# Kernel tuning notes

Measured on AMD Instinct MI355X. Metric: run time of the kernel, lower is better.

## Reference

```python
import jax, jax.numpy as jnp
import numpy as np

B, T, A, P = 128, 128, 16, 4
D, H, Q, QI, V = 256, 512, 128, 512, 64
NUM_TRICKS = 13
SIGNAL_PHASE = 1
# static phase routing: contiguous blocks of T/P positions per phase (phase_mask buffer)
PHASE_ID = (np.arange(T) * P // T).astype(np.int32)
_DECAY = 0.6
_nt_left = NUM_TRICKS - np.arange(NUM_TRICKS, dtype=np.float32)
P_SIGNAL = ((1.0 - _DECAY) / (1.0 - _DECAY ** _nt_left)).astype(np.float32)


def setup_inputs() -> dict:
    key = jax.random.key(0)
    ks = jax.random.split(key, 12)
    a = jax.random.randint(ks[0], (B, T, A, 3), 0, V, dtype=jnp.int32)
    pad = (jax.random.uniform(ks[1], (B, T, A)) < 0.3) & (jnp.arange(A) >= 1)
    valid_actions = jnp.where(pad[..., None], -1, a)
    phase = jnp.broadcast_to(jnp.asarray(PHASE_ID), (B, T)).astype(jnp.int32)
    trick = jax.random.randint(ks[2], (B, T), 0, NUM_TRICKS, dtype=jnp.int32)
    backbone_embed = jax.random.normal(ks[3], (B, T, QI), jnp.float32)
    s = lambda k, shape, fan: jax.random.normal(k, shape, jnp.float32) / np.float32(np.sqrt(fan))
    return dict(
        backbone_embed=backbone_embed, valid_actions=valid_actions, phase=phase, trick=trick,
        emb0=s(ks[4], (V, D), D), emb1=s(ks[5], (V, D), D), emb2=s(ks[6], (V, D), D),
        ln_g=jnp.ones((D,), jnp.float32), ln_b=jnp.zeros((D,), jnp.float32),
        kW1=s(ks[7], (P, D, H), D), kb1=jnp.zeros((P, H), jnp.float32),
        kW2=s(ks[8], (P, H, H), H), kb2=jnp.zeros((P, H), jnp.float32),
        kW3=s(ks[9], (P, H, Q), H), kb3=jnp.zeros((P, Q), jnp.float32),
        qW=s(ks[10], (P, QI, Q), QI), qb=jnp.zeros((P, Q), jnp.float32),
    )


def _forward(backbone_embed, valid_actions, phase, trick,
             emb0, emb1, emb2, ln_g, ln_b,
             kW1, kb1, kW2, kb2, kW3, kb3, qW, qb):
    pid = PHASE_ID  # static (T,) routing -> gather per-position phase params (same math as mask gather/scatter)
    idx = jnp.clip(valid_actions, 0, V - 1)
    x = emb0[idx[..., 0]] + emb1[idx[..., 1]] + emb2[idx[..., 2]]  # (B,T,A,D) action embed
    mu = jnp.mean(x, -1, keepdims=True)
    var = jnp.var(x, -1, keepdims=True)
    x = (x - mu) * jax.lax.rsqrt(var + 1e-5) * ln_g + ln_b  # key LayerNorm
    # phase-branched key MLP (BranchedFF over MLP)
    h = jax.nn.relu(jnp.einsum('btad,tdh->btah', x, kW1[pid]) + kb1[pid][None, :, None, :])
    h = jax.nn.relu(jnp.einsum('btah,thg->btag', h, kW2[pid]) + kb2[pid][None, :, None, :])
    keyv = jnp.einsum('btah,thq->btaq', h, kW3[pid]) + kb3[pid][None, :, None, :]  # (B,T,A,Q)
    # phase-branched query Linear (BranchedFF over Linear)
    query = jnp.einsum('btd,tdq->btq', backbone_embed, qW[pid]) + qb[pid][None]  # (B,T,Q)
    attn = jnp.einsum('btq,btaq->bta', query, keyv) / np.float32(np.sqrt(Q))
    invalid = valid_actions[..., 0] == -1
    attn = jnp.where(invalid, -jnp.inf, attn)
    # no-signal log-weight
    n_valid = jnp.sum(~invalid, -1).astype(attn.dtype)  # (B,T)
    p_s = jnp.asarray(P_SIGNAL)[trick]
    wgt = jnp.log(jnp.maximum((1.0 - p_s) / p_s * (n_valid - 1.0), 1e-5))
    wgt = jnp.where(n_valid == 1.0, 0.0, wgt)
    attn = attn.at[..., 0].add(jnp.where(phase == SIGNAL_PHASE, wgt, 0.0))
    return jax.nn.log_softmax(attn, axis=-1)


def reference(backbone_embed, valid_actions, phase, trick,
              emb0, emb1, emb2, ln_g, ln_b,
              kW1, kb1, kW2, kb2, kW3, kb3, qW, qb):
    return _forward(backbone_embed, valid_actions, phase, trick,
                    emb0, emb1, emb2, ln_g, ln_b,
                    kW1, kb1, kW2, kb2, kW3, kb3, qW, qb)
```

## Files before the change

### kernel.cpp

```cpp
#include <hip/hip_runtime.h>
#include <hip/hip_bf16.h>
#include <cmath>

constexpr int Bc = 128, Tc = 128, Ac = 16;
constexpr int Dc = 256, Hc = 512, Qc = 128, QIc = 512, Vc = 64, NTk = 13;
constexpr float NEG_BIG = -1e30f;
constexpr float ACT_SCALE = 16.f;
constexpr float ACC_SCALE = 1.f / 256.f;
constexpr float ACC_TO_ACT = 1.f / 16.f;

typedef unsigned int uint;
typedef uint uint2v __attribute__((ext_vector_type(2)));
typedef float f32x4 __attribute__((ext_vector_type(4)));

#define MFMA16F8(a, b, c) __builtin_amdgcn_mfma_f32_16x16x32_fp8_fp8(a, b, c, 0, 0, 0)

__device__ __forceinline__ long long u2ll(uint2v v) {
  union { uint2v u; long long l; } x;
  x.u = v;
  return x.l;
}
__device__ __forceinline__ unsigned short f2bfu(float f) {
  __hip_bfloat16 h = __float2bfloat16(f);
  return *(unsigned short*)&h;
}
__device__ __forceinline__ float bf2f(short s) {
  return __uint_as_float(((unsigned)(unsigned short)s) << 16);
}
__device__ __forceinline__ uint pack4_fp8(float a, float b, float c, float d) {
  uint v = 0;
  v = __builtin_amdgcn_cvt_pk_fp8_f32(a, b, v, 0);
  v = __builtin_amdgcn_cvt_pk_fp8_f32(c, d, v, 1);
  return v;
}

__global__ void transform_all(const float* __restrict__ kW1, const float* __restrict__ kW2,
                              const float* __restrict__ kW3, const float* __restrict__ qW,
                              uint2v* __restrict__ kW1f, uint2v* __restrict__ kW2f,
                              uint2v* __restrict__ kW3f, uint2v* __restrict__ qWf) {
  int gid = blockIdx.x * 256 + threadIdx.x;
  const float* W;
  uint2v* dst;
  int NT, KC, N, local;
  if (gid < 65536) {
    W = kW1; dst = kW1f; NT = 32; KC = 8; N = 512; local = gid;
  } else if (gid < 196608) {
    W = kW2; dst = kW2f; NT = 32; KC = 16; N = 512; local = gid - 65536;
  } else if (gid < 229376) {
    W = kW3; dst = kW3f; NT = 8; KC = 16; N = 128; local = gid - 196608;
  } else {
    W = qW; dst = qWf; NT = 8; KC = 16; N = 128; local = gid - 229376;
  }
  int lane = local & 63;
  int frag = local >> 6;
  int kc = frag % KC;
  int rest = frag / KC;
  int nt = rest % NT;
  int p = rest / NT;
  int K = KC * 32;
  int n = nt * 16 + (lane & 15);
  int k0 = kc * 32 + (lane >> 4) * 8;
  const float* src = W + ((size_t)p * K + k0) * N + n;
  float f[8];
#pragma unroll
  for (int j = 0; j < 8; ++j) f[j] = src[(size_t)j * N] * ACT_SCALE;
  uint2v v;
  v.x = pack4_fp8(f[0], f[1], f[2], f[3]);
  v.y = pack4_fp8(f[4], f[5], f[6], f[7]);
  dst[local] = v;
}

template <int KC, int WT, int AT, bool RELU, int OUTMODE, int SIN, int SOUT>
__device__ __forceinline__ void layer16(
    const char* __restrict__ aB, void* __restrict__ o0,
    const uint2v* __restrict__ Wf, const float* __restrict__ bias,
    int wt0, int lane) {
  const int c = lane & 15, q = lane >> 4;
  const char* ap = aB + c * SIN + q * 8;

  f32x4 acc[WT][AT];
#pragma unroll
  for (int wt = 0; wt < WT; ++wt)
#pragma unroll
    for (int at = 0; at < AT; ++at)
#pragma unroll
      for (int r = 0; r < 4; ++r) acc[wt][at][r] = 0.f;

#pragma unroll 1
  for (int kc = 0; kc < KC; ++kc) {
    uint2v bf[AT];
#pragma unroll
    for (int at = 0; at < AT; ++at)
      bf[at] = *(const uint2v*)(ap + at * 16 * SIN + kc * 32);
#pragma unroll
    for (int wt = 0; wt < WT; ++wt) {
      const uint2v* wk = Wf + ((size_t)(wt0 + wt) * KC + kc) * 64;
      uint2v wv = wk[lane];
      long long ww = u2ll(wv);
#pragma unroll
      for (int at = 0; at < AT; ++at)
        acc[wt][at] = MFMA16F8(ww, u2ll(bf[at]), acc[wt][at]);
    }
  }

#pragma unroll
  for (int wt = 0; wt < WT; ++wt) {
    const int nb = (wt0 + wt) * 16 + 4 * q;
    float4 bv = *(const float4*)(bias + nb);
#pragma unroll
    for (int at = 0; at < AT; ++at) {
      const int row = at * 16 + c;
      if (OUTMODE == 0) {
        float s0 = fmaf(acc[wt][at][0], ACC_TO_ACT, bv.x * ACT_SCALE);
        float s1 = fmaf(acc[wt][at][1], ACC_TO_ACT, bv.y * ACT_SCALE);
        float s2 = fmaf(acc[wt][at][2], ACC_TO_ACT, bv.z * ACT_SCALE);
        float s3 = fmaf(acc[wt][at][3], ACC_TO_ACT, bv.w * ACT_SCALE);
        if (RELU) {
          s0 = fmaxf(s0, 0.f); s1 = fmaxf(s1, 0.f);
          s2 = fmaxf(s2, 0.f); s3 = fmaxf(s3, 0.f);
        }
        *(uint*)((char*)o0 + row * SOUT + nb) = pack4_fp8(s0, s1, s2, s3);
      } else if (OUTMODE == 1) {
        float s0 = fmaf(acc[wt][at][0], ACC_SCALE, bv.x);
        float s1 = fmaf(acc[wt][at][1], ACC_SCALE, bv.y);
        float s2 = fmaf(acc[wt][at][2], ACC_SCALE, bv.z);
        float s3 = fmaf(acc[wt][at][3], ACC_SCALE, bv.w);
        uint2v u;
        u.x = ((uint)f2bfu(s1) << 16) | f2bfu(s0);
        u.y = ((uint)f2bfu(s3) << 16) | f2bfu(s2);
        *(uint2v*)((short*)o0 + row * SOUT + nb) = u;
      } else {
        if (c < 4) {
          float4 st;
          st.x = fmaf(acc[wt][at][0], ACC_SCALE, bv.x);
          st.y = fmaf(acc[wt][at][1], ACC_SCALE, bv.y);
          st.z = fmaf(acc[wt][at][2], ACC_SCALE, bv.z);
          st.w = fmaf(acc[wt][at][3], ACC_SCALE, bv.w);
          *(float4*)((float*)o0 + c * SOUT + nb) = st;
        }
      }
    }
  }
}

constexpr int SX = 280;
constexpr int SH = 536;
constexpr int SKV = 136;
constexpr int SQY = 132;

__global__ __launch_bounds__(1024, 8) void policy_main(
    const float* __restrict__ be, const int* __restrict__ va,
    const int* __restrict__ phase, const int* __restrict__ trick,
    const float* __restrict__ emb0, const float* __restrict__ emb1,
    const float* __restrict__ emb2, const float* __restrict__ ln_g,
    const float* __restrict__ ln_b,
    const float* __restrict__ kb1, const float* __restrict__ kb2,
    const float* __restrict__ kb3, const float* __restrict__ qb,
    const uint2v* __restrict__ kW1f, const uint2v* __restrict__ kW2f,
    const uint2v* __restrict__ kW3f, const uint2v* __restrict__ qWf,
    float* __restrict__ out) {
  __shared__ __align__(16) char bufA[64 * SH];
  __shared__ __align__(16) char bufB[64 * SH];
  __shared__ __align__(16) char beAb[16 * SH];
  __shared__ __align__(16) float QYs[4 * SQY];
  __shared__ float attn_s[64];
  __shared__ int inval_s[64];
  __shared__ int ph_s[4], tr_s[4];

  char* Xs = bufA;
  char* H2 = bufA;
  char* H1 = bufB;
  short* KV = (short*)bufB;

  const int tid = threadIdx.x;
  const int w = tid >> 6, lane = tid & 63;
  const int p = blockIdx.x & 3;
  const int g = blockIdx.x >> 2;
  const int b = g >> 3;
  const int t0 = p * 32 + (g & 7) * 4;
  const int bt0 = b * Tc + t0;

  if (tid < 64) {
    inval_s[tid] = (va[((size_t)bt0 * Ac + tid) * 3] == -1);
  } else if (tid < 68) {
    ph_s[tid - 64] = phase[bt0 + tid - 64];
  } else if (tid < 72) {
    tr_s[tid - 68] = trick[bt0 + tid - 68];
  }
  if (tid < 256) {
    int tok = tid >> 6, d0 = (tid & 63) * 8;
    const float* bp = be + ((size_t)bt0 + tok) * QIc + d0;
    uint2v v8;
    v8.x = pack4_fp8(bp[0] * ACT_SCALE, bp[1] * ACT_SCALE, bp[2] * ACT_SCALE, bp[3] * ACT_SCALE);
    v8.y = pack4_fp8(bp[4] * ACT_SCALE, bp[5] * ACT_SCALE, bp[6] * ACT_SCALE, bp[7] * ACT_SCALE);
    *(uint2v*)(beAb + tok * SH + d0) = v8;
  }
  {
    const int r = tid >> 4, part = tid & 15, d0 = part * 16;
    const int* vp = va + ((size_t)bt0 * Ac + r) * 3;
    int i0 = min(max(vp[0], 0), Vc - 1);
    int i1 = min(max(vp[1], 0), Vc - 1);
    int i2 = min(max(vp[2], 0), Vc - 1);
    const float4* e0 = (const float4*)(emb0 + i0 * Dc + d0);
    const float4* e1 = (const float4*)(emb1 + i1 * Dc + d0);
    const float4* e2 = (const float4*)(emb2 + i2 * Dc + d0);
    float xv[16];
    float sum = 0.f, ss = 0.f;
#pragma unroll
    for (int j = 0; j < 4; ++j) {
      float4 v0 = e0[j], v1 = e1[j], v2 = e2[j];
      float4 v;
      v.x = v0.x + v1.x + v2.x; v.y = v0.y + v1.y + v2.y;
      v.z = v0.z + v1.z + v2.z; v.w = v0.w + v1.w + v2.w;
      xv[j * 4 + 0] = v.x; xv[j * 4 + 1] = v.y; xv[j * 4 + 2] = v.z; xv[j * 4 + 3] = v.w;
      sum += v.x + v.y + v.z + v.w;
      ss += v.x * v.x + v.y * v.y + v.z * v.z + v.w * v.w;
    }
    sum += __shfl_xor(sum, 1); sum += __shfl_xor(sum, 2);
    sum += __shfl_xor(sum, 4); sum += __shfl_xor(sum, 8);
    ss += __shfl_xor(ss, 1);   ss += __shfl_xor(ss, 2);
    ss += __shfl_xor(ss, 4);   ss += __shfl_xor(ss, 8);
    const float mu = sum / (float)Dc;
    const float rstd = rsqrtf(ss / (float)Dc - mu * mu + 1e-5f);
    float y[16];
#pragma unroll
    for (int j = 0; j < 16; ++j) {
      int d = d0 + j;
      y[j] = ((xv[j] - mu) * rstd * ln_g[d] + ln_b[d]) * ACT_SCALE;
    }
    uint2v v8;
    v8.x = pack4_fp8(y[0], y[1], y[2], y[3]);
    v8.y = pack4_fp8(y[4], y[5], y[6], y[7]);
    *(uint2v*)(Xs + r * SX + d0) = v8;
    v8.x = pack4_fp8(y[8], y[9], y[10], y[11]);
    v8.y = pack4_fp8(y[12], y[13], y[14], y[15]);
    *(uint2v*)(Xs + r * SX + d0 + 8) = v8;
  }
  __syncthreads();

  layer16<8, 2, 4, true, 0, SX, SH>(Xs, H1, kW1f + (size_t)p * 32 * 8 * 64,
                                    kb1 + p * Hc, w * 2, lane);
  __syncthreads();

  layer16<16, 2, 4, true, 0, SH, SH>(H1, H2, kW2f + (size_t)p * 32 * 16 * 64,
                                     kb2 + p * Hc, w * 2, lane);
  __syncthreads();

  if (w < 8) {
    layer16<16, 1, 4, false, 1, SH, SKV>(H2, KV, kW3f + (size_t)p * 8 * 16 * 64,
                                         kb3 + p * Qc, w, lane);
  } else {
    layer16<16, 1, 1, false, 2, SH, SQY>(beAb, QYs, qWf + (size_t)p * 8 * 16 * 64,
                                         qb + p * Qc, w - 8, lane);
  }
  __syncthreads();

  {
    const int r = tid >> 4, part = tid & 15, tok = r >> 4;
    const short* kp = KV + r * SKV + part * 8;
    const float* qp = QYs + tok * SQY + part * 8;
    float s = 0.f;
#pragma unroll
    for (int j = 0; j < 8; ++j) s += bf2f(kp[j]) * qp[j];
    s += __shfl_xor(s, 1); s += __shfl_xor(s, 2);
    s += __shfl_xor(s, 4); s += __shfl_xor(s, 8);
    if (part == 0) attn_s[r] = s * 0.08838834764831845f;
  }
  __syncthreads();

  if (tid < 4) {
    const int tok = tid;
    const int bt = bt0 + tok;
    float av[Ac];
    int nv = 0;
#pragma unroll
    for (int a = 0; a < Ac; ++a) {
      int iv = inval_s[tok * Ac + a];
      nv += iv ? 0 : 1;
      av[a] = iv ? NEG_BIG : attn_s[tok * Ac + a];
    }
    if (ph_s[tok] == 1) {
      const int nt = NTk - tr_s[tok];
      float dp = 1.f;
      for (int i = 0; i < nt; ++i) dp *= 0.6f;
      const float ps = 0.4f / (1.f - dp);
      float wgt = (nv == 1) ? 0.f : logf(fmaxf((1.f - ps) / ps * ((float)nv - 1.f), 1e-5f));
      av[0] += wgt;
    }
    float m = NEG_BIG;
#pragma unroll
    for (int a = 0; a < Ac; ++a) m = fmaxf(m, av[a]);
    float s = 0.f;
#pragma unroll
    for (int a = 0; a < Ac; ++a) s += expf(av[a] - m);
    const float lse = logf(s) + m;
#pragma unroll
    for (int a = 0; a < Ac; ++a)
      out[bt * Ac + a] = inval_s[tok * Ac + a] ? NEG_BIG : (av[a] - lse);
  }
}

extern "C" void kernel_launch(void* const* d_in, const int* in_sizes, int n_in,
                              void* d_out, int out_size, void* d_ws, size_t ws_size,
                              hipStream_t stream) {
  const float* be   = (const float*)d_in[0];
  const int*   va   = (const int*)d_in[1];
  const int*   ph   = (const int*)d_in[2];
  const int*   tr   = (const int*)d_in[3];
  const float* emb0 = (const float*)d_in[4];
  const float* emb1 = (const float*)d_in[5];
  const float* emb2 = (const float*)d_in[6];
  const float* lng  = (const float*)d_in[7];
  const float* lnb  = (const float*)d_in[8];
  const float* kW1  = (const float*)d_in[9];
  const float* kb1  = (const float*)d_in[10];
  const float* kW2  = (const float*)d_in[11];
  const float* kb2  = (const float*)d_in[12];
  const float* kW3  = (const float*)d_in[13];
  const float* kb3  = (const float*)d_in[14];
  const float* qW   = (const float*)d_in[15];
  const float* qb   = (const float*)d_in[16];
  float* out = (float*)d_out;

  uint2v* kW1f = (uint2v*)d_ws;
  uint2v* kW2f = kW1f + 65536;
  uint2v* kW3f = kW2f + 131072;
  uint2v* qWf  = kW3f + 32768;

  transform_all<<<262144 / 256, 256, 0, stream>>>(kW1, kW2, kW3, qW, kW1f, kW2f, kW3f, qWf);

  policy_main<<<4096, 1024, 0, stream>>>(be, va, ph, tr, emb0, emb1, emb2, lng, lnb,
                                         kb1, kb2, kb3, qb, kW1f, kW2f, kW3f, qWf, out);
}
```

Before: 341.9 us.

## Switch FP8 GEMMs to 16x16x128 scaled MFMA with swizzled LDS and 512-thread blocks

Replaces the 16x16x32 fp8 MFMA with the gfx950 scaled 16x16x128 f8f6f4 MFMA, using neutral scales. The weight pre-transform now packs 32-byte fragments per lane, and LDS activation rows are XOR-swizzled by row parity with adjusted strides. Blocks shrink to 512 threads with 4 output tiles per wave, and the query projection runs on all waves after the key projection instead of on separate waves. The aim is fewer MFMA issues and fewer loop iterations per K, at the cost of more registers per wave and a serialised query layer.

```diff
diff --git a/kernel.cpp b/kernel.cpp
--- a/kernel.cpp
+++ b/kernel.cpp
@@ -11,15 +11,12 @@
 
 typedef unsigned int uint;
 typedef uint uint2v __attribute__((ext_vector_type(2)));
+typedef int i32x8 __attribute__((ext_vector_type(8)));
 typedef float f32x4 __attribute__((ext_vector_type(4)));
 
-#define MFMA16F8(a, b, c) __builtin_amdgcn_mfma_f32_16x16x32_fp8_fp8(a, b, c, 0, 0, 0)
-
-__device__ __forceinline__ long long u2ll(uint2v v) {
-  union { uint2v u; long long l; } x;
-  x.u = v;
-  return x.l;
-}
+#define MFMA128(a, b, c) __builtin_amdgcn_mfma_scale_f32_16x16x128_f8f6f4( \
+    (a), (b), (c), 0, 0, 0, 0x7F7F7F7F, 0, 0x7F7F7F7F)
+
 __device__ __forceinline__ unsigned short f2bfu(float f) {
   __hip_bfloat16 h = __float2bfloat16(f);
   return *(unsigned short*)&h;
@@ -36,47 +33,51 @@
 
 __global__ void transform_all(const float* __restrict__ kW1, const float* __restrict__ kW2,
                               const float* __restrict__ kW3, const float* __restrict__ qW,
-                              uint2v* __restrict__ kW1f, uint2v* __restrict__ kW2f,
-                              uint2v* __restrict__ kW3f, uint2v* __restrict__ qWf) {
+                              int* __restrict__ kW1f, int* __restrict__ kW2f,
+                              int* __restrict__ kW3f, int* __restrict__ qWf) {
   int gid = blockIdx.x * 256 + threadIdx.x;
   const float* W;
-  uint2v* dst;
+  int* dst;
   int NT, KC, N, local;
-  if (gid < 65536) {
-    W = kW1; dst = kW1f; NT = 32; KC = 8; N = 512; local = gid;
-  } else if (gid < 196608) {
-    W = kW2; dst = kW2f; NT = 32; KC = 16; N = 512; local = gid - 65536;
-  } else if (gid < 229376) {
-    W = kW3; dst = kW3f; NT = 8; KC = 16; N = 128; local = gid - 196608;
+  if (gid < 16384) {
+    W = kW1; dst = kW1f; NT = 32; KC = 2; N = 512; local = gid;
+  } else if (gid < 49152) {
+    W = kW2; dst = kW2f; NT = 32; KC = 4; N = 512; local = gid - 16384;
+  } else if (gid < 57344) {
+    W = kW3; dst = kW3f; NT = 8; KC = 4; N = 128; local = gid - 49152;
   } else {
-    W = qW; dst = qWf; NT = 8; KC = 16; N = 128; local = gid - 229376;
+    W = qW; dst = qWf; NT = 8; KC = 4; N = 128; local = gid - 57344;
   }
   int lane = local & 63;
   int frag = local >> 6;
   int kc = frag % KC;
   int rest = frag / KC;
   int nt = rest % NT;
-  int p = rest / NT;
-  int K = KC * 32;
+  int pp = rest / NT;
+  int K = KC * 128;
   int n = nt * 16 + (lane & 15);
-  int k0 = kc * 32 + (lane >> 4) * 8;
-  const float* src = W + ((size_t)p * K + k0) * N + n;
-  float f[8];
-#pragma unroll
-  for (int j = 0; j < 8; ++j) f[j] = src[(size_t)j * N] * ACT_SCALE;
-  uint2v v;
-  v.x = pack4_fp8(f[0], f[1], f[2], f[3]);
-  v.y = pack4_fp8(f[4], f[5], f[6], f[7]);
-  dst[local] = v;
-}
-
-template <int KC, int WT, int AT, bool RELU, int OUTMODE, int SIN, int SOUT>
-__device__ __forceinline__ void layer16(
+  int k0 = kc * 128 + (lane >> 4) * 32;
+  const float* src = W + ((size_t)pp * K + k0) * N + n;
+  i32x8 v;
+#pragma unroll
+  for (int jj = 0; jj < 8; ++jj) {
+    float f0 = src[(size_t)(4 * jj + 0) * N] * ACT_SCALE;
+    float f1 = src[(size_t)(4 * jj + 1) * N] * ACT_SCALE;
+    float f2 = src[(size_t)(4 * jj + 2) * N] * ACT_SCALE;
+    float f3 = src[(size_t)(4 * jj + 3) * N] * ACT_SCALE;
+    v[jj] = (int)pack4_fp8(f0, f1, f2, f3);
+  }
+  *(i32x8*)(dst + (size_t)local * 8) = v;
+}
+
+template <int KC, int WT, int AT, bool RELU, int OUTMODE, int SIN, int SOUT, int CMASK>
+__device__ __forceinline__ void layer128(
     const char* __restrict__ aB, void* __restrict__ o0,
-    const uint2v* __restrict__ Wf, const float* __restrict__ bias,
+    const int* __restrict__ Wfi, const float* __restrict__ bias,
     int wt0, int lane) {
   const int c = lane & 15, q = lane >> 4;
-  const char* ap = aB + c * SIN + q * 8;
+  const int sw = (c & 1) << 4;
+  const char* ap = aB + (c & CMASK) * SIN + q * 32;
 
   f32x4 acc[WT][AT];
 #pragma unroll
@@ -88,18 +89,23 @@
 
 #pragma unroll 1
   for (int kc = 0; kc < KC; ++kc) {
-    uint2v bf[AT];
-#pragma unroll
-    for (int at = 0; at < AT; ++at)
-      bf[at] = *(const uint2v*)(ap + at * 16 * SIN + kc * 32);
+    i32x8 bfr[AT];
+#pragma unroll
+    for (int at = 0; at < AT; ++at) {
+      const char* pa = ap + at * 16 * SIN + kc * 128;
+      uint4 u0 = *(const uint4*)(pa + sw);
+      uint4 u1 = *(const uint4*)(pa + (16 ^ sw));
+      i32x8 bv;
+      bv[0] = (int)u0.x; bv[1] = (int)u0.y; bv[2] = (int)u0.z; bv[3] = (int)u0.w;
+      bv[4] = (int)u1.x; bv[5] = (int)u1.y; bv[6] = (int)u1.z; bv[7] = (int)u1.w;
+      bfr[at] = bv;
+    }
 #pragma unroll
     for (int wt = 0; wt < WT; ++wt) {
-      const uint2v* wk = Wf + ((size_t)(wt0 + wt) * KC + kc) * 64;
-      uint2v wv = wk[lane];
-      long long ww = u2ll(wv);
+      const i32x8 wv = *(const i32x8*)(Wfi + ((size_t)((wt0 + wt) * KC + kc)) * 512 + lane * 8);
 #pragma unroll
       for (int at = 0; at < AT; ++at)
-        acc[wt][at] = MFMA16F8(ww, u2ll(bf[at]), acc[wt][at]);
+        acc[wt][at] = MFMA128(wv, bfr[at], acc[wt][at]);
     }
   }
 
@@ -119,7 +125,7 @@
           s0 = fmaxf(s0, 0.f); s1 = fmaxf(s1, 0.f);
           s2 = fmaxf(s2, 0.f); s3 = fmaxf(s3, 0.f);
         }
-        *(uint*)((char*)o0 + row * SOUT + nb) = pack4_fp8(s0, s1, s2, s3);
+        *(uint*)((char*)o0 + row * SOUT + (nb ^ sw)) = pack4_fp8(s0, s1, s2, s3);
       } else if (OUTMODE == 1) {
         float s0 = fmaf(acc[wt][at][0], ACC_SCALE, bv.x);
         float s1 = fmaf(acc[wt][at][1], ACC_SCALE, bv.y);
@@ -143,12 +149,12 @@
   }
 }
 
-constexpr int SX = 280;
-constexpr int SH = 536;
+constexpr int SX = 288;
+constexpr int SH = 544;
 constexpr int SKV = 136;
 constexpr int SQY = 132;
 
-__global__ __launch_bounds__(1024, 8) void policy_main(
+__global__ __launch_bounds__(512, 4) void policy_main(
     const float* __restrict__ be, const int* __restrict__ va,
     const int* __restrict__ phase, const int* __restrict__ trick,
     const float* __restrict__ emb0, const float* __restrict__ emb1,
@@ -156,12 +162,12 @@
     const float* __restrict__ ln_b,
     const float* __restrict__ kb1, const float* __restrict__ kb2,
     const float* __restrict__ kb3, const float* __restrict__ qb,
-    const uint2v* __restrict__ kW1f, const uint2v* __restrict__ kW2f,
-    const uint2v* __restrict__ kW3f, const uint2v* __restrict__ qWf,
+    const int* __restrict__ kW1f, const int* __restrict__ kW2f,
+    const int* __restrict__ kW3f, const int* __restrict__ qWf,
     float* __restrict__ out) {
   __shared__ __align__(16) char bufA[64 * SH];
   __shared__ __align__(16) char bufB[64 * SH];
-  __shared__ __align__(16) char beAb[16 * SH];
+  __shared__ __align__(16) char beAb[4 * SH];
   __shared__ __align__(16) float QYs[4 * SQY];
   __shared__ float attn_s[64];
   __shared__ int inval_s[64];
@@ -173,7 +179,8 @@
   short* KV = (short*)bufB;
 
   const int tid = threadIdx.x;
-  const int w = tid >> 6, lane = tid & 63;
+  const int lane = tid & 63;
+  const int wu = __builtin_amdgcn_readfirstlane(tid >> 6);
   const int p = blockIdx.x & 3;
   const int g = blockIdx.x >> 2;
   const int b = g >> 3;
@@ -187,16 +194,19 @@
   } else if (tid < 72) {
     tr_s[tid - 68] = trick[bt0 + tid - 68];
   }
-  if (tid < 256) {
-    int tok = tid >> 6, d0 = (tid & 63) * 8;
-    const float* bp = be + ((size_t)bt0 + tok) * QIc + d0;
-    uint2v v8;
-    v8.x = pack4_fp8(bp[0] * ACT_SCALE, bp[1] * ACT_SCALE, bp[2] * ACT_SCALE, bp[3] * ACT_SCALE);
-    v8.y = pack4_fp8(bp[4] * ACT_SCALE, bp[5] * ACT_SCALE, bp[6] * ACT_SCALE, bp[7] * ACT_SCALE);
-    *(uint2v*)(beAb + tok * SH + d0) = v8;
+  if (tid < 128) {
+    const int tok = tid >> 5, li = tid & 31;
+    const float4* bp4 = (const float4*)(be + ((size_t)(bt0 + tok)) * QIc + li * 16);
+    float4 a0 = bp4[0], a1 = bp4[1], a2 = bp4[2], a3 = bp4[3];
+    uint4 v;
+    v.x = pack4_fp8(a0.x * ACT_SCALE, a0.y * ACT_SCALE, a0.z * ACT_SCALE, a0.w * ACT_SCALE);
+    v.y = pack4_fp8(a1.x * ACT_SCALE, a1.y * ACT_SCALE, a1.z * ACT_SCALE, a1.w * ACT_SCALE);
+    v.z = pack4_fp8(a2.x * ACT_SCALE, a2.y * ACT_SCALE, a2.z * ACT_SCALE, a2.w * ACT_SCALE);
+    v.w = pack4_fp8(a3.x * ACT_SCALE, a3.y * ACT_SCALE, a3.z * ACT_SCALE, a3.w * ACT_SCALE);
+    *(uint4*)(beAb + tok * SH + ((li * 16) ^ ((tok & 1) << 4))) = v;
   }
   {
-    const int r = tid >> 4, part = tid & 15, d0 = part * 16;
+    const int r = tid >> 3, part = tid & 7, d0 = part * 32;
     const int* vp = va + ((size_t)bt0 * Ac + r) * 3;
     int i0 = min(max(vp[0], 0), Vc - 1);
     int i1 = min(max(vp[1], 0), Vc - 1);
@@ -204,10 +214,10 @@
     const float4* e0 = (const float4*)(emb0 + i0 * Dc + d0);
     const float4* e1 = (const float4*)(emb1 + i1 * Dc + d0);
     const float4* e2 = (const float4*)(emb2 + i2 * Dc + d0);
-    float xv[16];
+    float xv[32];
     float sum = 0.f, ss = 0.f;
 #pragma unroll
-    for (int j = 0; j < 4; ++j) {
+    for (int j = 0; j < 8; ++j) {
       float4 v0 = e0[j], v1 = e1[j], v2 = e2[j];
       float4 v;
       v.x = v0.x + v1.x + v2.x; v.y = v0.y + v1.y + v2.y;
@@ -216,54 +226,59 @@
       sum += v.x + v.y + v.z + v.w;
       ss += v.x * v.x + v.y * v.y + v.z * v.z + v.w * v.w;
     }
-    sum += __shfl_xor(sum, 1); sum += __shfl_xor(sum, 2);
-    sum += __shfl_xor(sum, 4); sum += __shfl_xor(sum, 8);
-    ss += __shfl_xor(ss, 1);   ss += __shfl_xor(ss, 2);
-    ss += __shfl_xor(ss, 4);   ss += __shfl_xor(ss, 8);
+    sum += __shfl_xor(sum, 1); sum += __shfl_xor(sum, 2); sum += __shfl_xor(sum, 4);
+    ss += __shfl_xor(ss, 1);   ss += __shfl_xor(ss, 2);   ss += __shfl_xor(ss, 4);
     const float mu = sum / (float)Dc;
     const float rstd = rsqrtf(ss / (float)Dc - mu * mu + 1e-5f);
-    float y[16];
-#pragma unroll
-    for (int j = 0; j < 16; ++j) {
-      int d = d0 + j;
-      y[j] = ((xv[j] - mu) * rstd * ln_g[d] + ln_b[d]) * ACT_SCALE;
-    }
-    uint2v v8;
-    v8.x = pack4_fp8(y[0], y[1], y[2], y[3]);
-    v8.y = pack4_fp8(y[4], y[5], y[6], y[7]);
-    *(uint2v*)(Xs + r * SX + d0) = v8;
-    v8.x = pack4_fp8(y[8], y[9], y[10], y[11]);
-    v8.y = pack4_fp8(y[12], y[13], y[14], y[15]);
-    *(uint2v*)(Xs + r * SX + d0 + 8) = v8;
-  }
-  __syncthreads();
-
-  layer16<8, 2, 4, true, 0, SX, SH>(Xs, H1, kW1f + (size_t)p * 32 * 8 * 64,
-                                    kb1 + p * Hc, w * 2, lane);
-  __syncthreads();
-
-  layer16<16, 2, 4, true, 0, SH, SH>(H1, H2, kW2f + (size_t)p * 32 * 16 * 64,
-                                     kb2 + p * Hc, w * 2, lane);
-  __syncthreads();
-
-  if (w < 8) {
-    layer16<16, 1, 4, false, 1, SH, SKV>(H2, KV, kW3f + (size_t)p * 8 * 16 * 64,
-                                         kb3 + p * Qc, w, lane);
-  } else {
-    layer16<16, 1, 1, false, 2, SH, SQY>(beAb, QYs, qWf + (size_t)p * 8 * 16 * 64,
-                                         qb + p * Qc, w - 8, lane);
-  }
+    uint dw[8];
+#pragma unroll
+    for (int j = 0; j < 8; ++j) {
+      float4 gg = *(const float4*)(ln_g + d0 + 4 * j);
+      float4 bb = *(const float4*)(ln_b + d0 + 4 * j);
+      float y0 = ((xv[4 * j + 0] - mu) * rstd * gg.x + bb.x) * ACT_SCALE;
+      float y1 = ((xv[4 * j + 1] - mu) * rstd * gg.y + bb.y) * ACT_SCALE;
+      float y2 = ((xv[4 * j + 2] - mu) * rstd * gg.z + bb.z) * ACT_SCALE;
+      float y3 = ((xv[4 * j + 3] - mu) * rstd * gg.w + bb.w) * ACT_SCALE;
+      dw[j] = pack4_fp8(y0, y1, y2, y3);
+    }
+    uint4 lo, hi;
+    lo.x = dw[0]; lo.y = dw[1]; lo.z = dw[2]; lo.w = dw[3];
+    hi.x = dw[4]; hi.y = dw[5]; hi.z = dw[6]; hi.w = dw[7];
+    const int swr = (r & 1) << 4;
+    *(uint4*)(Xs + r * SX + (d0 ^ swr)) = lo;
+    *(uint4*)(Xs + r * SX + ((d0 + 16) ^ swr)) = hi;
+  }
+  __syncthreads();
+
+  layer128<2, 4, 4, true, 0, SX, SH, 15>(Xs, H1, kW1f + (size_t)p * 32768,
+                                         kb1 + p * Hc, wu * 4, lane);
+  __syncthreads();
+
+  layer128<4, 4, 4, true, 0, SH, SH, 15>(H1, H2, kW2f + (size_t)p * 65536,
+                                         kb2 + p * Hc, wu * 4, lane);
+  __syncthreads();
+
+  layer128<4, 1, 4, false, 1, SH, SKV, 15>(H2, (void*)KV, kW3f + (size_t)p * 16384,
+                                           kb3 + p * Qc, wu, lane);
+  layer128<4, 1, 1, false, 2, SH, SQY, 3>(beAb, (void*)QYs, qWf + (size_t)p * 16384,
+                                          qb + p * Qc, wu, lane);
   __syncthreads();
 
   {
-    const int r = tid >> 4, part = tid & 15, tok = r >> 4;
-    const short* kp = KV + r * SKV + part * 8;
-    const float* qp = QYs + tok * SQY + part * 8;
+    const int r = tid >> 3, part = tid & 7, tok = r >> 4;
+    const uint2v* kpu = (const uint2v*)(KV + r * SKV + part * 16);
+    const float4* qp4 = (const float4*)(QYs + tok * SQY + part * 16);
     float s = 0.f;
 #pragma unroll
-    for (int j = 0; j < 8; ++j) s += bf2f(kp[j]) * qp[j];
-    s += __shfl_xor(s, 1); s += __shfl_xor(s, 2);
-    s += __shfl_xor(s, 4); s += __shfl_xor(s, 8);
+    for (int j = 0; j < 4; ++j) {
+      uint2v kk = kpu[j];
+      float4 qq = qp4[j];
+      s += bf2f((short)(kk.x & 0xffff)) * qq.x;
+      s += bf2f((short)(kk.x >> 16)) * qq.y;
+      s += bf2f((short)(kk.y & 0xffff)) * qq.z;
+      s += bf2f((short)(kk.y >> 16)) * qq.w;
+    }
+    s += __shfl_xor(s, 1); s += __shfl_xor(s, 2); s += __shfl_xor(s, 4);
     if (part == 0) attn_s[r] = s * 0.08838834764831845f;
   }
   __syncthreads();
@@ -322,13 +337,13 @@
   const float* qb   = (const float*)d_in[16];
   float* out = (float*)d_out;
 
-  uint2v* kW1f = (uint2v*)d_ws;
-  uint2v* kW2f = kW1f + 65536;
-  uint2v* kW3f = kW2f + 131072;
-  uint2v* qWf  = kW3f + 32768;
-
-  transform_all<<<262144 / 256, 256, 0, stream>>>(kW1, kW2, kW3, qW, kW1f, kW2f, kW3f, qWf);
-
-  policy_main<<<4096, 1024, 0, stream>>>(be, va, ph, tr, emb0, emb1, emb2, lng, lnb,
-                                         kb1, kb2, kb3, qb, kW1f, kW2f, kW3f, qWf, out);
-}
+  int* kW1f = (int*)d_ws;
+  int* kW2f = kW1f + 131072;
+  int* kW3f = kW2f + 262144;
+  int* qWf  = kW3f + 65536;
+
+  transform_all<<<256, 256, 0, stream>>>(kW1, kW2, kW3, qW, kW1f, kW2f, kW3f, qWf);
+
+  policy_main<<<4096, 512, 0, stream>>>(be, va, ph, tr, emb0, emb1, emb2, lng, lnb,
+                                        kb1, kb2, kb3, qb, kW1f, kW2f, kW3f, qWf, out);
+}
```

After: 370.7 us. 8.4% more time.
